# Kernel tuning notes

Hardware: AMD Instinct MI355X
Metric: run time of the kernel (lower is better)

Reference implementation:

```python
import jax, jax.numpy as jnp
import numpy as np

N_NODES = 100000
N_EDGES = 1250000
N_FEAT = 128
NHID = 64
NUM_GRAPHS = 256


def setup_inputs() -> dict:
    key = jax.random.key(0)
    ks = jax.random.split(key, 12)
    sc = lambda fan_in: 1.414 * (6.0 / fan_in) ** 0.5  # rough xavier-ish scale
    inp = {
        "x": jax.random.normal(ks[0], (N_NODES, N_FEAT), dtype=jnp.float32),
        "edge_attr": jax.random.uniform(ks[1], (N_EDGES, 5), dtype=jnp.float32),
        "W_e1": jax.random.normal(ks[2], (5, NHID), dtype=jnp.float32) * sc(5),
        "b_e1": jnp.zeros((NHID,), jnp.float32),
        "W_e2": jax.random.normal(ks[3], (NHID, NHID), dtype=jnp.float32) * sc(NHID),
        "b_e2": jnp.zeros((NHID,), jnp.float32),
        "W_e3": jax.random.normal(ks[4], (NHID, 1), dtype=jnp.float32) * sc(NHID),
        "b_e3": jnp.zeros((1,), jnp.float32),
        "W_g": jax.random.normal(ks[5], (N_FEAT, NHID), dtype=jnp.float32) * sc(N_FEAT),
        "b_g": jnp.zeros((NHID,), jnp.float32),
        "W_b1": jax.random.normal(ks[6], (NHID, NHID), dtype=jnp.float32) * sc(NHID),
        "b_b1": jnp.zeros((NHID,), jnp.float32),
        "W_b2": jax.random.normal(ks[7], (NHID, 1), dtype=jnp.float32) * sc(NHID),
        "b_b2": jnp.zeros((1,), jnp.float32),
        "edge_index": jax.random.randint(ks[8], (2, N_EDGES), 0, N_NODES, dtype=jnp.int64 if jax.config.jax_enable_x64 else jnp.int32),
        "batch": jnp.sort(jax.random.randint(ks[9], (N_NODES,), 0, NUM_GRAPHS, dtype=jnp.int64 if jax.config.jax_enable_x64 else jnp.int32)),
    }
    return inp


def _forward(x, edge_attr, W_e1, b_e1, W_e2, b_e2, W_e3, b_e3, W_g, b_g,
             W_b1, b_b1, W_b2, b_b2, edge_index, batch):
    N = x.shape[0]
    # edge MLP -> scalar weight per edge, then final ReLU (F.relu in forward)
    h = jax.nn.relu(edge_attr @ W_e1 + b_e1)
    h = jax.nn.relu(h @ W_e2 + b_e2)
    edge_w = jax.nn.relu((h @ W_e3 + b_e3)[:, 0])  # [E]

    row, col = edge_index[0], edge_index[1]
    # add self-loops with weight 1 (PyG GCNConv default)
    loop = jnp.arange(N, dtype=row.dtype)
    row_f = jnp.concatenate([row, loop])
    col_f = jnp.concatenate([col, loop])
    w_f = jnp.concatenate([edge_w, jnp.ones((N,), edge_w.dtype)])

    # symmetric normalization D^{-1/2} A_hat D^{-1/2}
    deg = jax.ops.segment_sum(w_f, col_f, num_segments=N)
    dinv = jnp.where(deg > 0, jax.lax.rsqrt(jnp.where(deg > 0, deg, 1.0)), 0.0)
    norm = dinv[row_f] * w_f * dinv[col_f]  # [E+N]

    xw = x @ W_g  # [N, nhid]
    agg = jax.ops.segment_sum(xw[row_f] * norm[:, None], col_f, num_segments=N)
    node = jax.nn.relu(agg + b_g)  # dropout is identity in eval mode

    pooled = jax.ops.segment_sum(node, batch, num_segments=NUM_GRAPHS)  # [G, nhid]
    z = jax.nn.relu(pooled @ W_b1 + b_b1)
    logits = z @ W_b2 + b_b2  # [G, 1]
    return logits


def reference(x, edge_attr, W_e1, b_e1, W_e2, b_e2, W_e3, b_e3, W_g, b_g,
              W_b1, b_b1, W_b2, b_b2, edge_index, batch):
    return _forward(x, edge_attr, W_e1, b_e1, W_e2, b_e2, W_e3, b_e3, W_g, b_g,
                    W_b1, b_b1, W_b2, b_b2, edge_index, batch)
```

## Files before the change

### kernel.cpp

```cpp
#include <hip/hip_runtime.h>
#include <hip/hip_bf16.h>

#define N_NODES 100000
#define N_EDGES 1250000
#define N_FEAT 128
#define NHID 64
#define NUM_GRAPHS 256
#define NB_SCAN 98

typedef __attribute__((ext_vector_type(8))) short short8;
typedef __attribute__((ext_vector_type(16))) float float16;

static __device__ __forceinline__ short f2bf(float x) {
    __hip_bfloat16 b = __float2bfloat16(x);
    return *reinterpret_cast<short*>(&b);
}
static __device__ __forceinline__ float bf2f(short s) {
    __hip_bfloat16 b = *reinterpret_cast<__hip_bfloat16*>(&s);
    return __bfloat162float(b);
}

__global__ void k0_init(int* __restrict__ cnt, float* __restrict__ pooled) {
    int i = blockIdx.x * blockDim.x + threadIdx.x;
    if (i < N_NODES) cnt[i] = 0;
    if (i < NUM_GRAPHS * NHID) pooled[i] = 0.0f;
}

__global__ __launch_bounds__(256) void k1_edge_mlp(
    const float* __restrict__ ea, const float* __restrict__ W1,
    const float* __restrict__ b1, const float* __restrict__ W2,
    const float* __restrict__ b2, const float* __restrict__ W3,
    const float* __restrict__ b3, const int* __restrict__ eidx,
    float* __restrict__ edge_w, int* __restrict__ cnt)
{
    const int lane = threadIdx.x & 63;
    const int l31 = lane & 31;
    const int h = lane >> 5;
    const int wslot = blockIdx.x * 4 + (threadIdx.x >> 6);
    const float b3v = b3[0];

    short8 a1hi[2], a1lo[2];
    #pragma unroll
    for (int t = 0; t < 2; ++t)
        #pragma unroll
        for (int j = 0; j < 8; ++j) {
            int k = 8 * h + j;
            float v = (k < 5) ? W1[k * NHID + t * 32 + l31] : 0.0f;
            short hi = f2bf(v);
            a1hi[t][j] = hi;
            a1lo[t][j] = f2bf(v - bf2f(hi));
        }

    float b1r[2][16];
    #pragma unroll
    for (int t = 0; t < 2; ++t)
        #pragma unroll
        for (int r = 0; r < 16; ++r)
            b1r[t][r] = b1[t * 32 + (r & 3) + 8 * (r >> 2) + 4 * h];

    short8 afrag[2][4];
    #pragma unroll
    for (int t = 0; t < 2; ++t)
        #pragma unroll
        for (int kk = 0; kk < 4; ++kk)
            #pragma unroll
            for (int j = 0; j < 8; ++j) {
                int k = kk * 16 + h * 8 + j;
                afrag[t][kk][j] = f2bf(W2[k * NHID + t * 32 + l31]);
            }

    float b2r[2][16], w3r[2][16];
    #pragma unroll
    for (int t = 0; t < 2; ++t)
        #pragma unroll
        for (int r = 0; r < 16; ++r) {
            int hid = t * 32 + (r & 3) + 8 * (r >> 2) + 4 * h;
            b2r[t][r] = b2[hid];
            w3r[t][r] = W3[hid];
        }

    const int NCHUNK = (N_EDGES + 31) / 32;
    for (int chunk = wslot; chunk < NCHUNK; chunk += gridDim.x * 4) {
        int e = chunk * 32 + l31;
        bool valid = e < N_EDGES;
        int ec = valid ? e : (N_EDGES - 1);

        short8 behi, belo;
        #pragma unroll
        for (int j = 0; j < 8; ++j) {
            float v = (h == 0 && j < 5) ? ea[ec * 5 + j] : 0.0f;
            short hi = f2bf(v);
            behi[j] = hi;
            belo[j] = f2bf(v - bf2f(hi));
        }

        float16 acc1a, acc1b;
        #pragma unroll
        for (int r = 0; r < 16; ++r) { acc1a[r] = b1r[0][r]; acc1b[r] = b1r[1][r]; }
        acc1a = __builtin_amdgcn_mfma_f32_32x32x16_bf16(a1hi[0], behi, acc1a, 0, 0, 0);
        acc1a = __builtin_amdgcn_mfma_f32_32x32x16_bf16(a1hi[0], belo, acc1a, 0, 0, 0);
        acc1a = __builtin_amdgcn_mfma_f32_32x32x16_bf16(a1lo[0], behi, acc1a, 0, 0, 0);
        acc1b = __builtin_amdgcn_mfma_f32_32x32x16_bf16(a1hi[1], behi, acc1b, 0, 0, 0);
        acc1b = __builtin_amdgcn_mfma_f32_32x32x16_bf16(a1hi[1], belo, acc1b, 0, 0, 0);
        acc1b = __builtin_amdgcn_mfma_f32_32x32x16_bf16(a1lo[1], behi, acc1b, 0, 0, 0);
        #pragma unroll
        for (int r = 0; r < 16; ++r) {
            acc1a[r] = fmaxf(acc1a[r], 0.0f);
            acc1b[r] = fmaxf(acc1b[r], 0.0f);
        }

        short8 bf2v[4];
        #pragma unroll
        for (int kk = 0; kk < 4; ++kk) {
            #pragma unroll
            for (int j2 = 0; j2 < 4; ++j2) {
                float lv, hv;
                if (kk >> 1) { lv = acc1b[j2 + 8 * (kk & 1)]; hv = acc1b[j2 + 8 * (kk & 1) + 4]; }
                else         { lv = acc1a[j2 + 8 * (kk & 1)]; hv = acc1a[j2 + 8 * (kk & 1) + 4]; }
                float send = h ? lv : hv;
                float recv = __shfl_xor(send, 32, 64);
                float jlo = h ? recv : lv;
                float jhi = h ? hv : recv;
                bf2v[kk][j2] = f2bf(jlo);
                bf2v[kk][4 + j2] = f2bf(jhi);
            }
        }

        float16 c0, c1;
        #pragma unroll
        for (int r = 0; r < 16; ++r) { c0[r] = b2r[0][r]; c1[r] = b2r[1][r]; }
        #pragma unroll
        for (int kk = 0; kk < 4; ++kk) {
            c0 = __builtin_amdgcn_mfma_f32_32x32x16_bf16(afrag[0][kk], bf2v[kk], c0, 0, 0, 0);
            c1 = __builtin_amdgcn_mfma_f32_32x32x16_bf16(afrag[1][kk], bf2v[kk], c1, 0, 0, 0);
        }

        float partial = 0.0f;
        #pragma unroll
        for (int r = 0; r < 16; ++r) {
            partial += fmaxf(c0[r], 0.0f) * w3r[0][r];
            partial += fmaxf(c1[r], 0.0f) * w3r[1][r];
        }
        float total = partial + __shfl_xor(partial, 32, 64);
        float w = fmaxf(total + b3v, 0.0f);

        if (h == 0 && valid) {
            edge_w[e] = w;
            if (w > 0.0f) atomicAdd(&cnt[eidx[N_EDGES + e]], 1);
        }
    }
}

__global__ __launch_bounds__(1024) void s1_blocksum(const int* __restrict__ cnt,
                                                    int* __restrict__ bsum) {
    __shared__ int sd[1024];
    int t = threadIdx.x;
    int i = blockIdx.x * 1024 + t;
    sd[t] = (i < N_NODES) ? cnt[i] : 0;
    __syncthreads();
    #pragma unroll
    for (int d = 512; d > 0; d >>= 1) {
        if (t < d) sd[t] += sd[t + d];
        __syncthreads();
    }
    if (t == 0) bsum[blockIdx.x] = sd[0];
}

__global__ void s2_scanbase(const int* __restrict__ bsum, int* __restrict__ bbase,
                            int* __restrict__ off) {
    if (threadIdx.x == 0 && blockIdx.x == 0) {
        int run = 0;
        for (int b = 0; b < NB_SCAN; ++b) { bbase[b] = run; run += bsum[b]; }
        off[N_NODES] = run;
    }
}

__global__ __launch_bounds__(1024) void s3_blockscan(const int* __restrict__ cnt,
                                                     const int* __restrict__ bbase,
                                                     int* __restrict__ off,
                                                     int* __restrict__ cur) {
    __shared__ int sd[1024];
    int t = threadIdx.x;
    int i = blockIdx.x * 1024 + t;
    int c = (i < N_NODES) ? cnt[i] : 0;
    sd[t] = c;
    __syncthreads();
    #pragma unroll
    for (int d = 1; d < 1024; d <<= 1) {
        int v = (t >= d) ? sd[t - d] : 0;
        __syncthreads();
        sd[t] += v;
        __syncthreads();
    }
    if (i < N_NODES) {
        int ex = sd[t] - c + bbase[blockIdx.x];
        off[i] = ex;
        cur[i] = ex;
    }
}

__global__ void k_place(const float* __restrict__ edge_w, const int* __restrict__ eidx,
                        int* __restrict__ cur, int2* __restrict__ recs) {
    int e = blockIdx.x * 256 + threadIdx.x;
    if (e >= N_EDGES) return;
    float w = edge_w[e];
    if (w <= 0.0f) return;
    int col = eidx[N_EDGES + e];
    int pos = atomicAdd(&cur[col], 1);
    recs[pos] = make_int2(eidx[e], __float_as_int(w));
}

__global__ void k_deg(const int* __restrict__ off, const int2* __restrict__ recs,
                      float* __restrict__ dinv) {
    int n = blockIdx.x * 256 + threadIdx.x;
    if (n >= N_NODES) return;
    int o0 = off[n], o1 = off[n + 1];
    float s = 1.0f;
    for (int j = o0; j < o1; ++j) s += __int_as_float(recs[j].y);
    dinv[n] = rsqrtf(s);
}

__global__ __launch_bounds__(256) void k3_xw(
    const float* __restrict__ x, const float* __restrict__ Wg,
    const float* __restrict__ dinv, float* __restrict__ xws)
{
    const int lane = threadIdx.x & 63;
    const int l31 = lane & 31;
    const int h = lane >> 5;
    const int wslot = blockIdx.x * 4 + (threadIdx.x >> 6);

    short8 bw[8][2];
    #pragma unroll
    for (int kk = 0; kk < 8; ++kk)
        #pragma unroll
        for (int u = 0; u < 2; ++u)
            #pragma unroll
            for (int j = 0; j < 8; ++j)
                bw[kk][u][j] = f2bf(Wg[(kk * 16 + 8 * h + j) * NHID + u * 32 + l31]);

    const int NC = N_NODES / 32;
    for (int chunk = wslot; chunk < NC; chunk += gridDim.x * 4) {
        int base = chunk * 32;
        const float* xrow = x + (size_t)(base + l31) * N_FEAT + 8 * h;

        float16 acc0, acc1;
        #pragma unroll
        for (int r = 0; r < 16; ++r) { acc0[r] = 0.0f; acc1[r] = 0.0f; }

        #pragma unroll
        for (int kk = 0; kk < 8; ++kk) {
            float4 p = *(const float4*)(xrow + kk * 16);
            float4 q = *(const float4*)(xrow + kk * 16 + 4);
            short8 af;
            af[0] = f2bf(p.x); af[1] = f2bf(p.y); af[2] = f2bf(p.z); af[3] = f2bf(p.w);
            af[4] = f2bf(q.x); af[5] = f2bf(q.y); af[6] = f2bf(q.z); af[7] = f2bf(q.w);
            acc0 = __builtin_amdgcn_mfma_f32_32x32x16_bf16(af, bw[kk][0], acc0, 0, 0, 0);
            acc1 = __builtin_amdgcn_mfma_f32_32x32x16_bf16(af, bw[kk][1], acc1, 0, 0, 0);
        }

        #pragma unroll
        for (int r = 0; r < 16; ++r) {
            int node = base + (r & 3) + 8 * (r >> 2) + 4 * h;
            float dv = dinv[node];
            xws[node * NHID + l31] = acc0[r] * dv;
            xws[node * NHID + 32 + l31] = acc1[r] * dv;
        }
    }
}

__global__ __launch_bounds__(256) void k4_gather_pool(
    const int* __restrict__ off, const int2* __restrict__ recs,
    const float* __restrict__ xws, const float* __restrict__ dinv,
    const float* __restrict__ bg, const int* __restrict__ batch,
    float* __restrict__ pooled)
{
    const int lane = threadIdx.x & 63;
    const int wv = blockIdx.x * 4 + (threadIdx.x >> 6);
    int n0 = wv * 8;
    if (n0 >= N_NODES) return;
    float bgl = bg[lane];
    float pacc = 0.0f;
    int curg = batch[n0];
    #pragma unroll
    for (int nn = 0; nn < 8; ++nn) {
        int n = n0 + nn;
        int g = batch[n];
        if (g != curg) {
            atomicAdd(&pooled[curg * NHID + lane], pacc);
            pacc = 0.0f;
            curg = g;
        }
        int o0 = off[n], o1 = off[n + 1];
        float acc = xws[(size_t)n * NHID + lane];
        if (o0 < o1) {
            int2 r = recs[o0];
            float gth = xws[(size_t)r.x * NHID + lane];
            for (int j = o0; j < o1 - 1; ++j) {
                int2 rn = recs[j + 1];
                float gn = xws[(size_t)rn.x * NHID + lane];
                acc = fmaf(__int_as_float(r.y), gth, acc);
                r = rn; gth = gn;
            }
            acc = fmaf(__int_as_float(r.y), gth, acc);
        }
        pacc += fmaxf(dinv[n] * acc + bgl, 0.0f);
    }
    atomicAdd(&pooled[curg * NHID + lane], pacc);
}

__global__ __launch_bounds__(64) void k6_final(
    const float* __restrict__ pooled, const float* __restrict__ Wb1,
    const float* __restrict__ bb1, const float* __restrict__ Wb2,
    const float* __restrict__ bb2, float* __restrict__ out) {
    __shared__ float p[NHID];
    int lane = threadIdx.x;
    int g = blockIdx.x;
    p[lane] = pooled[g * NHID + lane];
    __syncthreads();
    float z = bb1[lane];
    #pragma unroll
    for (int k = 0; k < NHID; ++k) z += p[k] * Wb1[k * NHID + lane];
    z = fmaxf(z, 0.0f) * Wb2[lane];
    #pragma unroll
    for (int off = 32; off > 0; off >>= 1)
        z += __shfl_down(z, off, 64);
    if (lane == 0) out[g] = z + bb2[0];
}

extern "C" void kernel_launch(void* const* d_in, const int* in_sizes, int n_in,
                              void* d_out, int out_size, void* d_ws, size_t ws_size,
                              hipStream_t stream) {
    const float* x        = (const float*)d_in[0];
    const float* ea       = (const float*)d_in[1];
    const float* W_e1     = (const float*)d_in[2];
    const float* b_e1     = (const float*)d_in[3];
    const float* W_e2     = (const float*)d_in[4];
    const float* b_e2     = (const float*)d_in[5];
    const float* W_e3     = (const float*)d_in[6];
    const float* b_e3     = (const float*)d_in[7];
    const float* W_g      = (const float*)d_in[8];
    const float* b_g      = (const float*)d_in[9];
    const float* W_b1     = (const float*)d_in[10];
    const float* b_b1     = (const float*)d_in[11];
    const float* W_b2     = (const float*)d_in[12];
    const float* b_b2     = (const float*)d_in[13];
    const int*   eidx     = (const int*)d_in[14];
    const int*   batch    = (const int*)d_in[15];
    float* out = (float*)d_out;

    char* wsb = (char*)d_ws;
    float* edge_w = (float*)wsb;
    int*   cnt    = (int*)(wsb + 4 * 1250048);
    int*   off    = (int*)(wsb + 4 * 1350080);
    int*   cur    = (int*)(wsb + 4 * 1450112);
    int*   bsum   = (int*)(wsb + 4 * 1550144);
    int*   bbase  = (int*)(wsb + 4 * 1550272);
    float* dinv   = (float*)(wsb + 4 * 1550400);
    float* pooled = (float*)(wsb + 4 * 1650432);
    int2*  recs   = (int2*)(wsb + 4 * 1666880);
    float* xws    = (float*)(wsb + 4 * 4166880);

    k0_init<<<dim3(391), dim3(256), 0, stream>>>(cnt, pooled);
    k1_edge_mlp<<<dim3(1024), dim3(256), 0, stream>>>(
        ea, W_e1, b_e1, W_e2, b_e2, W_e3, b_e3, eidx, edge_w, cnt);
    s1_blocksum<<<dim3(NB_SCAN), dim3(1024), 0, stream>>>(cnt, bsum);
    s2_scanbase<<<dim3(1), dim3(64), 0, stream>>>(bsum, bbase, off);
    s3_blockscan<<<dim3(NB_SCAN), dim3(1024), 0, stream>>>(cnt, bbase, off, cur);
    k_place<<<dim3((N_EDGES + 255) / 256), dim3(256), 0, stream>>>(edge_w, eidx, cur, recs);
    k_deg<<<dim3((N_NODES + 255) / 256), dim3(256), 0, stream>>>(off, recs, dinv);
    k3_xw<<<dim3(512), dim3(256), 0, stream>>>(x, W_g, dinv, xws);
    k4_gather_pool<<<dim3(3125), dim3(256), 0, stream>>>(off, recs, xws, dinv, b_g, batch, pooled);
    k6_final<<<dim3(NUM_GRAPHS), dim3(64), 0, stream>>>(pooled, W_b1, b_b1, W_b2, b_b2, out);
}
```

Measured before the change: 226.9 us.

## Prefetch edge attributes, pack bf16 shuffles, parallelize base scan, double MLP grid

In the edge MLP kernel, the next chunk's edge attributes are now loaded into registers before the current chunk is computed, so global load latency is hidden. ReLU is folded into the repacking step, and values are packed two bf16 per int before the cross-half shuffle, halving the number of shuffles. The single-thread serial block-base scan is replaced by a 128-thread shared-memory Hillis-Steele scan, and the edge MLP grid is doubled. Prefetching adds register pressure, which could lower occupancy.

```diff
diff --git a/kernel.cpp b/kernel.cpp
--- a/kernel.cpp
+++ b/kernel.cpp
@@ -10,6 +10,7 @@
 
 typedef __attribute__((ext_vector_type(8))) short short8;
 typedef __attribute__((ext_vector_type(16))) float float16;
+typedef __attribute__((ext_vector_type(4))) int int4v;
 
 static __device__ __forceinline__ short f2bf(float x) {
     __hip_bfloat16 b = __float2bfloat16(x);
@@ -18,6 +19,11 @@
 static __device__ __forceinline__ float bf2f(short s) {
     __hip_bfloat16 b = *reinterpret_cast<__hip_bfloat16*>(&s);
     return __bfloat162float(b);
+}
+static __device__ __forceinline__ int pk2(float a, float b) {
+    unsigned lo = (unsigned short)f2bf(a);
+    unsigned hi = (unsigned short)f2bf(b);
+    return (int)(lo | (hi << 16));
 }
 
 __global__ void k0_init(int* __restrict__ cnt, float* __restrict__ pooled) {
@@ -37,6 +43,7 @@
     const int l31 = lane & 31;
     const int h = lane >> 5;
     const int wslot = blockIdx.x * 4 + (threadIdx.x >> 6);
+    const int S = gridDim.x * 4;
     const float b3v = b3[0];
 
     short8 a1hi[2], a1lo[2];
@@ -80,15 +87,32 @@
         }
 
     const int NCHUNK = (N_EDGES + 31) / 32;
-    for (int chunk = wslot; chunk < NCHUNK; chunk += gridDim.x * 4) {
+
+    float pe[5] = {0.f, 0.f, 0.f, 0.f, 0.f};
+    if (wslot < NCHUNK && h == 0) {
+        int e = wslot * 32 + l31;
+        int ec = (e < N_EDGES) ? e : (N_EDGES - 1);
+        #pragma unroll
+        for (int j = 0; j < 5; ++j) pe[j] = ea[ec * 5 + j];
+    }
+
+    for (int chunk = wslot; chunk < NCHUNK; chunk += S) {
+        int nchunk = chunk + S;
+        float ne[5] = {0.f, 0.f, 0.f, 0.f, 0.f};
+        if (nchunk < NCHUNK && h == 0) {
+            int e2 = nchunk * 32 + l31;
+            int ec2 = (e2 < N_EDGES) ? e2 : (N_EDGES - 1);
+            #pragma unroll
+            for (int j = 0; j < 5; ++j) ne[j] = ea[ec2 * 5 + j];
+        }
+
         int e = chunk * 32 + l31;
         bool valid = e < N_EDGES;
-        int ec = valid ? e : (N_EDGES - 1);
 
         short8 behi, belo;
         #pragma unroll
         for (int j = 0; j < 8; ++j) {
-            float v = (h == 0 && j < 5) ? ea[ec * 5 + j] : 0.0f;
+            float v = (h == 0 && j < 5) ? pe[j] : 0.0f;
             short hi = f2bf(v);
             behi[j] = hi;
             belo[j] = f2bf(v - bf2f(hi));
@@ -103,27 +127,36 @@
         acc1b = __builtin_amdgcn_mfma_f32_32x32x16_bf16(a1hi[1], behi, acc1b, 0, 0, 0);
         acc1b = __builtin_amdgcn_mfma_f32_32x32x16_bf16(a1hi[1], belo, acc1b, 0, 0, 0);
         acc1b = __builtin_amdgcn_mfma_f32_32x32x16_bf16(a1lo[1], behi, acc1b, 0, 0, 0);
-        #pragma unroll
-        for (int r = 0; r < 16; ++r) {
-            acc1a[r] = fmaxf(acc1a[r], 0.0f);
-            acc1b[r] = fmaxf(acc1b[r], 0.0f);
-        }
 
         short8 bf2v[4];
         #pragma unroll
         for (int kk = 0; kk < 4; ++kk) {
-            #pragma unroll
-            for (int j2 = 0; j2 < 4; ++j2) {
-                float lv, hv;
-                if (kk >> 1) { lv = acc1b[j2 + 8 * (kk & 1)]; hv = acc1b[j2 + 8 * (kk & 1) + 4]; }
-                else         { lv = acc1a[j2 + 8 * (kk & 1)]; hv = acc1a[j2 + 8 * (kk & 1) + 4]; }
-                float send = h ? lv : hv;
-                float recv = __shfl_xor(send, 32, 64);
-                float jlo = h ? recv : lv;
-                float jhi = h ? hv : recv;
-                bf2v[kk][j2] = f2bf(jlo);
-                bf2v[kk][4 + j2] = f2bf(jhi);
+            float lv0, lv1, lv2, lv3, hv0, hv1, hv2, hv3;
+            if (kk >> 1) {
+                int o = 8 * (kk & 1);
+                lv0 = fmaxf(acc1b[o + 0], 0.f); lv1 = fmaxf(acc1b[o + 1], 0.f);
+                lv2 = fmaxf(acc1b[o + 2], 0.f); lv3 = fmaxf(acc1b[o + 3], 0.f);
+                hv0 = fmaxf(acc1b[o + 4], 0.f); hv1 = fmaxf(acc1b[o + 5], 0.f);
+                hv2 = fmaxf(acc1b[o + 6], 0.f); hv3 = fmaxf(acc1b[o + 7], 0.f);
+            } else {
+                int o = 8 * (kk & 1);
+                lv0 = fmaxf(acc1a[o + 0], 0.f); lv1 = fmaxf(acc1a[o + 1], 0.f);
+                lv2 = fmaxf(acc1a[o + 2], 0.f); lv3 = fmaxf(acc1a[o + 3], 0.f);
+                hv0 = fmaxf(acc1a[o + 4], 0.f); hv1 = fmaxf(acc1a[o + 5], 0.f);
+                hv2 = fmaxf(acc1a[o + 6], 0.f); hv3 = fmaxf(acc1a[o + 7], 0.f);
             }
+            int p_lv0 = pk2(lv0, lv1), p_lv1 = pk2(lv2, lv3);
+            int p_hv0 = pk2(hv0, hv1), p_hv1 = pk2(hv2, hv3);
+            int send0 = h ? p_lv0 : p_hv0;
+            int send1 = h ? p_lv1 : p_hv1;
+            int r0 = __shfl_xor(send0, 32, 64);
+            int r1 = __shfl_xor(send1, 32, 64);
+            int4v fi;
+            fi.x = h ? r0 : p_lv0;
+            fi.y = h ? r1 : p_lv1;
+            fi.z = h ? p_hv0 : r0;
+            fi.w = h ? p_hv1 : r1;
+            bf2v[kk] = __builtin_bit_cast(short8, fi);
         }
 
         float16 c0, c1;
@@ -148,6 +181,9 @@
             edge_w[e] = w;
             if (w > 0.0f) atomicAdd(&cnt[eidx[N_EDGES + e]], 1);
         }
+
+        #pragma unroll
+        for (int j = 0; j < 5; ++j) pe[j] = ne[j];
     }
 }
 
@@ -166,13 +202,23 @@
     if (t == 0) bsum[blockIdx.x] = sd[0];
 }
 
-__global__ void s2_scanbase(const int* __restrict__ bsum, int* __restrict__ bbase,
-                            int* __restrict__ off) {
-    if (threadIdx.x == 0 && blockIdx.x == 0) {
-        int run = 0;
-        for (int b = 0; b < NB_SCAN; ++b) { bbase[b] = run; run += bsum[b]; }
-        off[N_NODES] = run;
-    }
+__global__ __launch_bounds__(128) void s2_scanbase(const int* __restrict__ bsum,
+                                                   int* __restrict__ bbase,
+                                                   int* __restrict__ off) {
+    __shared__ int sd[128];
+    int t = threadIdx.x;
+    int v = (t < NB_SCAN) ? bsum[t] : 0;
+    sd[t] = v;
+    __syncthreads();
+    #pragma unroll
+    for (int d = 1; d < 128; d <<= 1) {
+        int u = (t >= d) ? sd[t - d] : 0;
+        __syncthreads();
+        sd[t] += u;
+        __syncthreads();
+    }
+    if (t < NB_SCAN) bbase[t] = sd[t] - v;
+    if (t == 127) off[N_NODES] = sd[127];
 }
 
 __global__ __launch_bounds__(1024) void s3_blockscan(const int* __restrict__ cnt,
@@ -361,10 +407,10 @@
     float* xws    = (float*)(wsb + 4 * 4166880);
 
     k0_init<<<dim3(391), dim3(256), 0, stream>>>(cnt, pooled);
-    k1_edge_mlp<<<dim3(1024), dim3(256), 0, stream>>>(
+    k1_edge_mlp<<<dim3(2048), dim3(256), 0, stream>>>(
         ea, W_e1, b_e1, W_e2, b_e2, W_e3, b_e3, eidx, edge_w, cnt);
     s1_blocksum<<<dim3(NB_SCAN), dim3(1024), 0, stream>>>(cnt, bsum);
-    s2_scanbase<<<dim3(1), dim3(64), 0, stream>>>(bsum, bbase, off);
+    s2_scanbase<<<dim3(1), dim3(128), 0, stream>>>(bsum, bbase, off);
     s3_blockscan<<<dim3(NB_SCAN), dim3(1024), 0, stream>>>(cnt, bbase, off, cur);
     k_place<<<dim3((N_EDGES + 255) / 256), dim3(256), 0, stream>>>(edge_w, eidx, cur, recs);
     k_deg<<<dim3((N_NODES + 255) / 256), dim3(256), 0, stream>>>(off, recs, dinv);
```

Measured after the change: 233.3 us. 1.03x slower.
